# Kernel tuning notes

Hardware: AMD Instinct MI355X
Metric: run time of the kernel (lower is better)

Reference implementation:

```python
import jax, jax.numpy as jnp
import numpy as np

B, L, H = 8, 2048, 1024

def setup_inputs() -> dict:
    key = jax.random.key(0)
    k1, k2, k3, k4 = jax.random.split(key, 4)
    inputs = jax.random.normal(k1, (B, L, H), dtype=jnp.float32)
    mask = jax.random.normal(k2, (B, L, L), dtype=jnp.float32) * 0.01
    W = jax.random.normal(k3, (H, H), dtype=jnp.float32) * (1.0 / np.sqrt(H))
    b = jax.random.normal(k4, (H,), dtype=jnp.float32) * 0.01
    return {"inputs": inputs, "mask": mask, "W": W, "b": b}

def reference(inputs, mask, W, b):
    # q = Linear(inputs): [B, L, H]
    q = jnp.einsum('blh,oh->blo', inputs, W) + b
    # u = q @ inputs^T: [B, L, L]  (no 1/sqrt(d) scaling)
    u = jnp.einsum('blh,bmh->blm', q, inputs)
    u = jax.nn.relu(u)  # relu=True
    a = jax.nn.softmax(u, axis=2)
    a = a + mask  # mask added AFTER softmax
    h = jnp.einsum('blm,bmh->blh', a, inputs)
    return (h, a)
```

## Files before the change

### kernel.cpp

```cpp
#include <hip/hip_runtime.h>

#define Bb 8
#define Ll 2048
#define Hh 1024

typedef __bf16 bf16;
typedef signed char i8;
typedef __attribute__((ext_vector_type(8))) __bf16 bf16x8;
typedef __attribute__((ext_vector_type(4))) __bf16 bf16x4;
typedef __attribute__((ext_vector_type(4))) float f32x4;
typedef __attribute__((ext_vector_type(4))) int i32x4;

#define RX 6.0f
#define RW 0.25f

__device__ __forceinline__ void gload16(const void* src, void* dst) {
  __builtin_amdgcn_global_load_lds(
      (const __attribute__((address_space(1))) void*)src,
      (__attribute__((address_space(3))) void*)dst, 16, 0, 0);
}

__device__ __forceinline__ i8 q8(float v, float inv_s) {
  float r = fminf(fmaxf(v * inv_s, -127.f), 127.f);
  return (i8)__float2int_rn(r);
}

__global__ __launch_bounds__(256) void split_x_k(
    const float* __restrict__ X, bf16* __restrict__ Xhi,
    i8* __restrict__ Xhi8, i8* __restrict__ Xlo8, bf16* __restrict__ XT) {
  __shared__ float tile[64][65];
  const int h0 = blockIdx.x << 6, l0 = blockIdx.y << 6, b = blockIdx.z;
  const int t = threadIdx.x;
  const int c = t & 63, r0 = t >> 6;
  const long base = ((long)b * Ll + l0) * Hh + h0;
  const float* Xb = X + base;
  bf16* XhiB = Xhi + base;
  i8* Xhi8B = Xhi8 + base;
  i8* Xlo8B = Xlo8 + base;
  const float ih = 127.f / RX, il = 127.f * 512.f / RX;
#pragma unroll
  for (int i = 0; i < 16; ++i) {
    int row = (i << 2) + r0;
    long o = (long)row * Hh + c;
    float x = Xb[o];
    bf16 hi = (bf16)x;
    float hf = (float)hi;
    XhiB[o] = hi;
    Xhi8B[o] = q8(hf, ih);
    Xlo8B[o] = q8(x - hf, il);
    tile[row][c] = x;
  }
  __syncthreads();
  bf16* XTB = XT + ((long)b * Hh + h0) * Ll + l0;
#pragma unroll
  for (int i = 0; i < 16; ++i) {
    int row = (i << 2) + r0;
    XTB[(long)row * Ll + c] = (bf16)tile[c][row];
  }
}

__global__ __launch_bounds__(256) void split_w_k(
    const float* __restrict__ W, bf16* __restrict__ Whi,
    i8* __restrict__ Whi8, i8* __restrict__ Wlo8) {
  int i = blockIdx.x * 256 + threadIdx.x;
  float4 v = ((const float4*)W)[i];
  const float ih = 127.f / RW, il = 127.f * 512.f / RW;
  float vv[4] = {v.x, v.y, v.z, v.w};
#pragma unroll
  for (int j = 0; j < 4; ++j) {
    float x = vv[j];
    bf16 hi = (bf16)x;
    float hf = (float)hi;
    Whi[i * 4 + j] = hi;
    Whi8[i * 4 + j] = q8(hf, ih);
    Wlo8[i * 4 + j] = q8(x - hf, il);
  }
}

template <int EPI, int MODE>
__global__ __launch_bounds__(256, 2) void gemm_nt(
    const bf16* __restrict__ Ahi, const i8* __restrict__ Ahi8,
    const i8* __restrict__ Alo8, const bf16* __restrict__ Bhi,
    const i8* __restrict__ Bhi8, const i8* __restrict__ Blo8, int N, int K,
    long sA_, long sB_, long sC_, float C8, float* __restrict__ outF,
    bf16* __restrict__ outQhi, i8* __restrict__ outQhi8,
    i8* __restrict__ outQlo8, const float* __restrict__ bias) {
  constexpr int LDSB = MODE ? 65536 : 32768;
  __shared__ char lds[LDSB];
  bf16* AH = (bf16*)lds;
  bf16* BH = (bf16*)(lds + 16384);
  char* AI = lds + 32768;
  char* BI = lds + 49152;

  const int b = blockIdx.z;
  const int m0 = blockIdx.y * 128;
  const int n0 = blockIdx.x * 128;
  const bf16* Ah = Ahi + (long)b * sA_ + (long)m0 * K;
  const bf16* Bh = Bhi + (long)b * sB_ + (long)n0 * K;

  const int t = threadIdx.x;
  const int lane = t & 63;
  const int w = t >> 6;
  const int wr = (w >> 1) * 64, wc = (w & 1) * 64;
  const int g = lane >> 4;
  const int fr = lane & 15;

  f32x4 acc[4][4];
  i32x4 acc8[4][4];
#pragma unroll
  for (int m = 0; m < 4; ++m)
#pragma unroll
    for (int n = 0; n < 4; ++n) {
      acc[m][n] = {0.f, 0.f, 0.f, 0.f};
      if constexpr (MODE) acc8[m][n] = {0, 0, 0, 0};
    }

  const bf16 *sAh[4], *sBh[4];
  const i8 *sA8[4], *sB8[4];
#pragma unroll
  for (int p = 0; p < 4; ++p) {
    int c = p * 256 + t;
    int row = c >> 3;
    int l = (c & 7) ^ (row & 7);
    sAh[p] = Ah + (long)row * K + l * 8;
    sBh[p] = Bh + (long)row * K + l * 8;
    if constexpr (MODE) {
      const i8* a8 = (l < 4) ? Ahi8 : Alo8;
      const i8* b8 = (l < 4) ? Bhi8 : Blo8;
      sA8[p] = a8 + (long)b * sA_ + ((long)(m0 + row)) * K + (l & 3) * 16;
      sB8[p] = b8 + (long)b * sB_ + ((long)(n0 + row)) * K + (l & 3) * 16;
    }
  }

  for (int kt = 0; kt < K; kt += 64) {
#pragma unroll
    for (int p = 0; p < 4; ++p) {
      const int d = (p * 256 + t) * 16;
      gload16(sAh[p] + kt, (char*)AH + d);
      gload16(sBh[p] + kt, (char*)BH + d);
      if constexpr (MODE) {
        gload16(sA8[p] + kt, AI + d);
        gload16(sB8[p] + kt, BI + d);
      }
    }
    __syncthreads();
#pragma unroll
    for (int ks = 0; ks < 2; ++ks) {
      bf16x8 ah[4], bh[4];
#pragma unroll
      for (int m = 0; m < 4; ++m) {
        int row = wr + m * 16 + fr;
        ah[m] = *(const bf16x8*)&AH[row * 64 + ((((ks << 2) | g) ^ (row & 7)) << 3)];
      }
#pragma unroll
      for (int n = 0; n < 4; ++n) {
        int row = wc + n * 16 + fr;
        bh[n] = *(const bf16x8*)&BH[row * 64 + ((((ks << 2) | g) ^ (row & 7)) << 3)];
      }
#pragma unroll
      for (int m = 0; m < 4; ++m)
#pragma unroll
        for (int n = 0; n < 4; ++n)
          acc[m][n] = __builtin_amdgcn_mfma_f32_16x16x32_bf16(ah[m], bh[n],
                                                              acc[m][n], 0, 0, 0);
    }
    if constexpr (MODE) {
      i32x4 ah8[4], al8[4], bh8[4], bl8[4];
#pragma unroll
      for (int m = 0; m < 4; ++m) {
        int row = wr + m * 16 + fr;
        ah8[m] = *(const i32x4*)(AI + row * 128 + ((g ^ (row & 7)) << 4));
        al8[m] = *(const i32x4*)(AI + row * 128 + (((4 | g) ^ (row & 7)) << 4));
      }
#pragma unroll
      for (int n = 0; n < 4; ++n) {
        int row = wc + n * 16 + fr;
        bh8[n] = *(const i32x4*)(BI + row * 128 + ((g ^ (row & 7)) << 4));
        bl8[n] = *(const i32x4*)(BI + row * 128 + (((4 | g) ^ (row & 7)) << 4));
      }
#pragma unroll
      for (int m = 0; m < 4; ++m)
#pragma unroll
        for (int n = 0; n < 4; ++n) {
          acc8[m][n] = __builtin_amdgcn_mfma_i32_16x16x64_i8(ah8[m], bl8[n],
                                                             acc8[m][n], 0, 0, 0);
          acc8[m][n] = __builtin_amdgcn_mfma_i32_16x16x64_i8(al8[m], bh8[n],
                                                             acc8[m][n], 0, 0, 0);
        }
    }
    __syncthreads();
  }

  const int crow0 = m0 + wr + (lane >> 4) * 4;
  const int ccol0 = n0 + wc + fr;
#pragma unroll
  for (int m = 0; m < 4; ++m)
#pragma unroll
    for (int n = 0; n < 4; ++n)
#pragma unroll
      for (int j = 0; j < 4; ++j) {
        const int r = crow0 + m * 16 + j;
        const int cc = ccol0 + n * 16;
        float v = acc[m][n][j];
        if constexpr (MODE) v += C8 * (float)acc8[m][n][j];
        const long off = (long)b * sC_ + (long)r * N + cc;
        if constexpr (EPI == 0) {
          v += bias[cc];
          bf16 hi = (bf16)v;
          outQhi[off] = hi;
          float hf = (float)hi;
          outQhi8[off] = q8(hf, 127.f / RX);
          outQlo8[off] = q8(v - hf, 127.f * 512.f / RX);
        } else if constexpr (EPI == 1) {
          outF[off] = v > 0.f ? v : 0.f;
        } else {
          outF[off] = v;
        }
      }
}

__global__ __launch_bounds__(256) void softmax_mask_k(
    float* __restrict__ U, const float* __restrict__ mask,
    bf16* __restrict__ Abf) {
  __shared__ float red[8];
  const long row = blockIdx.x;
  float* u = U + row * 2048;
  const float* mk = mask + row * 2048;
  bf16* ab = Abf + row * 2048;
  const int t = threadIdx.x;
  float4 v0 = *(const float4*)(u + t * 4);
  float4 v1 = *(const float4*)(u + 1024 + t * 4);
  float m = fmaxf(fmaxf(fmaxf(v0.x, v0.y), fmaxf(v0.z, v0.w)),
                  fmaxf(fmaxf(v1.x, v1.y), fmaxf(v1.z, v1.w)));
#pragma unroll
  for (int s = 32; s; s >>= 1) m = fmaxf(m, __shfl_xor(m, s));
  if ((t & 63) == 0) red[t >> 6] = m;
  __syncthreads();
  m = fmaxf(fmaxf(red[0], red[1]), fmaxf(red[2], red[3]));
  float e0 = __expf(v0.x - m), e1 = __expf(v0.y - m), e2 = __expf(v0.z - m),
        e3 = __expf(v0.w - m);
  float e4 = __expf(v1.x - m), e5 = __expf(v1.y - m), e6 = __expf(v1.z - m),
        e7 = __expf(v1.w - m);
  float s = ((e0 + e1) + (e2 + e3)) + ((e4 + e5) + (e6 + e7));
#pragma unroll
  for (int sh = 32; sh; sh >>= 1) s += __shfl_xor(s, sh);
  if ((t & 63) == 0) red[4 + (t >> 6)] = s;
  __syncthreads();
  s = (red[4] + red[5]) + (red[6] + red[7]);
  const float inv = 1.0f / s;
  float4 k0 = *(const float4*)(mk + t * 4);
  float4 k1 = *(const float4*)(mk + 1024 + t * 4);
  float4 a0 = {e0 * inv + k0.x, e1 * inv + k0.y, e2 * inv + k0.z,
               e3 * inv + k0.w};
  float4 a1 = {e4 * inv + k1.x, e5 * inv + k1.y, e6 * inv + k1.z,
               e7 * inv + k1.w};
  *(float4*)(u + t * 4) = a0;
  *(float4*)(u + 1024 + t * 4) = a1;
  bf16x4 b0 = {(bf16)a0.x, (bf16)a0.y, (bf16)a0.z, (bf16)a0.w};
  bf16x4 b1 = {(bf16)a1.x, (bf16)a1.y, (bf16)a1.z, (bf16)a1.w};
  *(bf16x4*)(ab + t * 4) = b0;
  *(bf16x4*)(ab + 1024 + t * 4) = b1;
}

extern "C" void kernel_launch(void* const* d_in, const int* in_sizes, int n_in,
                              void* d_out, int out_size, void* d_ws,
                              size_t ws_size, hipStream_t stream) {
  const float* X = (const float*)d_in[0];
  const float* mask = (const float*)d_in[1];
  const float* W = (const float*)d_in[2];
  const float* bias = (const float*)d_in[3];
  float* out_h = (float*)d_out;
  float* out_a = out_h + (size_t)Bb * Ll * Hh;

  const size_t NX = (size_t)Bb * Ll * Hh;
  const size_t NA = (size_t)Bb * Ll * Ll;
  const size_t NW = (size_t)Hh * Hh;
  bf16* Xhi = (bf16*)d_ws;
  bf16* XT = Xhi + NX;
  bf16* Qhi = XT + NX;
  bf16* Abf = Qhi + NX;
  bf16* Whi = Abf + NA;
  i8* Xhi8 = (i8*)(Whi + NW);
  i8* Xlo8 = Xhi8 + NX;
  i8* Qhi8 = Xlo8 + NX;
  i8* Qlo8 = Qhi8 + NX;
  i8* Whi8 = Qlo8 + NX;
  i8* Wlo8 = Whi8 + NW;

  const float C8_1 = (RX / 127.f) * (RW / 127.f) / 512.f;
  const float C8_2 = (RX / 127.f) * (RX / 127.f) / 512.f;

  split_x_k<<<dim3(Hh / 64, Ll / 64, Bb), 256, 0, stream>>>(X, Xhi, Xhi8,
                                                            Xlo8, XT);
  split_w_k<<<dim3((Hh * Hh / 4) / 256), 256, 0, stream>>>(W, Whi, Whi8, Wlo8);
  gemm_nt<0, 1><<<dim3(Hh / 128, (Bb * Ll) / 128, 1), 256, 0, stream>>>(
      Xhi, Xhi8, Xlo8, Whi, Whi8, Wlo8, Hh, Hh, 0, 0, 0, C8_1, nullptr, Qhi,
      Qhi8, Qlo8, bias);
  gemm_nt<1, 1><<<dim3(Ll / 128, Ll / 128, Bb), 256, 0, stream>>>(
      Qhi, Qhi8, Qlo8, Xhi, Xhi8, Xlo8, Ll, Hh, (long)Ll * Hh, (long)Ll * Hh,
      (long)Ll * Ll, C8_2, out_a, nullptr, nullptr, nullptr, nullptr);
  softmax_mask_k<<<dim3(Bb * Ll), 256, 0, stream>>>(out_a, mask, Abf);
  gemm_nt<2, 0><<<dim3(Hh / 128, Ll / 128, Bb), 256, 0, stream>>>(
      Abf, nullptr, nullptr, XT, nullptr, nullptr, Hh, Ll, (long)Ll * Ll,
      (long)Hh * Ll, (long)Ll * Hh, 0.f, out_h, nullptr, nullptr, nullptr,
      nullptr);
}
```

Baseline: 489.8 us.

## Double-buffer LDS tiles in gemm_nt to overlap global loads with MFMA

Doubles the shared-memory allocation so the next K-tile is prefetched with global_load_lds into the alternate buffer while the current tile is consumed by MFMAs, keeping one barrier per iteration. The goal is to hide global-to-LDS latency that the single-buffer load/sync/compute loop exposed. In the cost, the int8 split mode now needs 128KB of LDS, so its launch bound drops to one block per CU, and the bf16 mode uses 64KB per block. Any latency hiding that came from two co-resident blocks is lost in MODE=1.

Measured after the change: 551.1 us. 12.5% more time.

```diff
diff --git a/kernel.cpp b/kernel.cpp
--- a/kernel.cpp
+++ b/kernel.cpp
@@ -78,19 +78,15 @@
 }
 
 template <int EPI, int MODE>
-__global__ __launch_bounds__(256, 2) void gemm_nt(
+__global__ __launch_bounds__(256, MODE ? 1 : 2) void gemm_nt(
     const bf16* __restrict__ Ahi, const i8* __restrict__ Ahi8,
     const i8* __restrict__ Alo8, const bf16* __restrict__ Bhi,
     const i8* __restrict__ Bhi8, const i8* __restrict__ Blo8, int N, int K,
     long sA_, long sB_, long sC_, float C8, float* __restrict__ outF,
     bf16* __restrict__ outQhi, i8* __restrict__ outQhi8,
     i8* __restrict__ outQlo8, const float* __restrict__ bias) {
-  constexpr int LDSB = MODE ? 65536 : 32768;
-  __shared__ char lds[LDSB];
-  bf16* AH = (bf16*)lds;
-  bf16* BH = (bf16*)(lds + 16384);
-  char* AI = lds + 32768;
-  char* BI = lds + 49152;
+  constexpr int BUFB = MODE ? 65536 : 32768;
+  __shared__ char lds[2 * BUFB];
 
   const int b = blockIdx.z;
   const int m0 = blockIdx.y * 128;
@@ -132,18 +128,33 @@
     }
   }
 
-  for (int kt = 0; kt < K; kt += 64) {
+  auto STAGE = [&](int buf, int kt) {
+    char* base = lds + buf * BUFB;
 #pragma unroll
     for (int p = 0; p < 4; ++p) {
       const int d = (p * 256 + t) * 16;
-      gload16(sAh[p] + kt, (char*)AH + d);
-      gload16(sBh[p] + kt, (char*)BH + d);
+      gload16(sAh[p] + kt, base + d);
+      gload16(sBh[p] + kt, base + 16384 + d);
       if constexpr (MODE) {
-        gload16(sA8[p] + kt, AI + d);
-        gload16(sB8[p] + kt, BI + d);
-      }
-    }
-    __syncthreads();
+        gload16(sA8[p] + kt, base + 32768 + d);
+        gload16(sB8[p] + kt, base + 49152 + d);
+      }
+    }
+  };
+
+  STAGE(0, 0);
+  __syncthreads();
+  int cur = 0;
+
+  for (int kt = 0; kt < K; kt += 64) {
+    if (kt + 64 < K) STAGE(cur ^ 1, kt + 64);
+
+    char* base = lds + cur * BUFB;
+    bf16* AH = (bf16*)base;
+    bf16* BH = (bf16*)(base + 16384);
+    char* AI = base + 32768;
+    char* BI = base + 49152;
+
 #pragma unroll
     for (int ks = 0; ks < 2; ++ks) {
       bf16x8 ah[4], bh[4];
@@ -189,6 +200,7 @@
         }
     }
     __syncthreads();
+    cur ^= 1;
   }
 
   const int crow0 = m0 + wr + (lane >> 4) * 4;
```
